# Optimization experiments

Measured on AMD Instinct MI355X. Metric: run time of the kernel, lower is better.

Reference implementation:

```python
import jax, jax.numpy as jnp
import numpy as np

N_GROUPS = 8
TOPK_GROUPS = 4
TOPK = 8
ROUTE_SCALE = 2.5


def setup_inputs() -> dict:
    key = jax.random.key(0)
    k1, k2, k3 = jax.random.split(key, 3)
    x = jax.random.normal(k1, (8192, 7168), dtype=jnp.float32)
    weight = jax.random.normal(k2, (256, 7168), dtype=jnp.float32) * 0.02
    bias = jax.random.normal(k3, (256,), dtype=jnp.float32) * 0.02
    return {"x": x, "weight": weight, "bias": bias}


def reference(x, weight, bias):
    n_tokens = x.shape[0]
    n_experts = weight.shape[0]
    # router GEMM: [T, E]
    logits = jnp.einsum('td,ed->te', x, weight)
    scores = jax.nn.sigmoid(logits)  # score_func == 'sigmoid'
    original_scores = scores
    scores = scores + bias  # bias present since dim == 7168
    # group-limited routing: [T, G, E/G]
    scores_g = scores.reshape(n_tokens, N_GROUPS, -1)
    # bias is not None -> group score = sum of top-2 in each group
    group_scores = jnp.sum(jax.lax.top_k(scores_g, 2)[0], axis=-1)  # [T, G]
    _, grp_idx = jax.lax.top_k(group_scores, TOPK_GROUPS)  # [T, topk_groups]
    mask = jnp.sum(jax.nn.one_hot(grp_idx, N_GROUPS, dtype=scores.dtype), axis=1)  # [T, G]
    masked = (scores_g * mask[:, :, None]).reshape(n_tokens, n_experts)
    _, indices = jax.lax.top_k(masked, TOPK)  # [T, topk]
    weights = jnp.take_along_axis(original_scores, indices, axis=1)
    weights = weights / jnp.sum(weights, axis=-1, keepdims=True)  # sigmoid normalization
    weights = weights * ROUTE_SCALE
    return weights.astype(x.dtype), indices
```

## Files before the change

### kernel.cpp

```cpp
#include <hip/hip_runtime.h>
#include <math.h>

typedef _Float16 f16;
typedef f16 f16x4 __attribute__((ext_vector_type(4)));
typedef f16 f16x8 __attribute__((ext_vector_type(8)));
typedef float f32x4 __attribute__((ext_vector_type(4)));

#define TOKENS 8192
#define EXPERTS 256
#define KDIM 7168
#define BM 128
#define BN 256
#define BK 32
#define SPLITK 4
#define KCHUNK (KDIM / SPLITK)
#define NSTEP (KCHUNK / BK)
#define APAD 40

#define XSCALE 256.0f
#define WSCALE 4096.0f

__device__ __forceinline__ void cvt4(const float4 v, const float scale, f16x4* hi, f16x4* lo) {
  float a = v.x * scale, b = v.y * scale, c = v.z * scale, d = v.w * scale;
  f16 ha = (f16)a, hb = (f16)b, hc = (f16)c, hd = (f16)d;
  f16x4 h, l;
  h.x = ha; h.y = hb; h.z = hc; h.w = hd;
  l.x = (f16)(a - (float)ha);
  l.y = (f16)(b - (float)hb);
  l.z = (f16)(c - (float)hc);
  l.w = (f16)(d - (float)hd);
  *hi = h; *lo = l;
}

__global__ __launch_bounds__(512, 2) void router_gemm(const float* __restrict__ x,
                                                      const float* __restrict__ w,
                                                      float* __restrict__ logits) {
  __shared__ f16 Ah[BM][APAD], Al[BM][APAD];
  __shared__ f16 Bh[BN][APAD], Bl[BN][APAD];

  const int tid = threadIdx.x;
  const int mtile = blockIdx.x >> 2;
  const int ks = blockIdx.x & 3;
  const int m0 = mtile * BM;
  const int k0 = ks * KCHUNK;

  const int lane = tid & 63;
  const int wv = tid >> 6;
  const int wm = wv >> 2;
  const int wn = wv & 3;
  const int fr = lane & 15;
  const int fq = lane >> 4;

  f32x4 acc0[4][4];
  f32x4 accX[4][4];
#pragma unroll
  for (int i = 0; i < 4; ++i)
#pragma unroll
    for (int j = 0; j < 4; ++j) {
      acc0[i][j] = (f32x4){0.f, 0.f, 0.f, 0.f};
      accX[i][j] = (f32x4){0.f, 0.f, 0.f, 0.f};
    }

  const int arow0 = tid >> 3;
  const int ac4 = tid & 7;
  const float* xp = x + (size_t)(m0 + arow0) * KDIM + k0 + ac4 * 4;
  const float* wp = w + (size_t)arow0 * KDIM + k0 + ac4 * 4;

  float4 ra[2], rb[4];
#pragma unroll
  for (int i = 0; i < 2; ++i) ra[i] = *(const float4*)(xp + (size_t)(64 * i) * KDIM);
#pragma unroll
  for (int i = 0; i < 4; ++i) rb[i] = *(const float4*)(wp + (size_t)(64 * i) * KDIM);

  for (int step = 0; step < NSTEP; ++step) {
    __syncthreads();
#pragma unroll
    for (int i = 0; i < 2; ++i) {
      f16x4 h, l;
      cvt4(ra[i], XSCALE, &h, &l);
      const int row = arow0 + 64 * i;
      *(f16x4*)&Ah[row][ac4 * 4] = h;
      *(f16x4*)&Al[row][ac4 * 4] = l;
    }
#pragma unroll
    for (int i = 0; i < 4; ++i) {
      f16x4 h, l;
      cvt4(rb[i], WSCALE, &h, &l);
      const int row = arow0 + 64 * i;
      *(f16x4*)&Bh[row][ac4 * 4] = h;
      *(f16x4*)&Bl[row][ac4 * 4] = l;
    }
    __syncthreads();
    if (step + 1 < NSTEP) {
      const float* xq = xp + (step + 1) * BK;
      const float* wq = wp + (step + 1) * BK;
#pragma unroll
      for (int i = 0; i < 2; ++i) ra[i] = *(const float4*)(xq + (size_t)(64 * i) * KDIM);
#pragma unroll
      for (int i = 0; i < 4; ++i) rb[i] = *(const float4*)(wq + (size_t)(64 * i) * KDIM);
    }
    f16x8 fa_h[4], fa_l[4], fb_h[4], fb_l[4];
#pragma unroll
    for (int m = 0; m < 4; ++m) {
      const int row = wm * 64 + m * 16 + fr;
      fa_h[m] = *(const f16x8*)&Ah[row][fq * 8];
      fa_l[m] = *(const f16x8*)&Al[row][fq * 8];
    }
#pragma unroll
    for (int n = 0; n < 4; ++n) {
      const int row = wn * 64 + n * 16 + fr;
      fb_h[n] = *(const f16x8*)&Bh[row][fq * 8];
      fb_l[n] = *(const f16x8*)&Bl[row][fq * 8];
    }
#pragma unroll
    for (int m = 0; m < 4; ++m)
#pragma unroll
      for (int n = 0; n < 4; ++n) {
        acc0[m][n] = __builtin_amdgcn_mfma_f32_16x16x32_f16(fa_h[m], fb_h[n], acc0[m][n], 0, 0, 0);
        accX[m][n] = __builtin_amdgcn_mfma_f32_16x16x32_f16(fa_h[m], fb_l[n], accX[m][n], 0, 0, 0);
        accX[m][n] = __builtin_amdgcn_mfma_f32_16x16x32_f16(fa_l[m], fb_h[n], accX[m][n], 0, 0, 0);
      }
  }

  constexpr float inv = 1.0f / (XSCALE * WSCALE);
#pragma unroll
  for (int m = 0; m < 4; ++m)
#pragma unroll
    for (int n = 0; n < 4; ++n)
#pragma unroll
      for (int j = 0; j < 4; ++j) {
        const int row = m0 + wm * 64 + m * 16 + fq * 4 + j;
        const int col = wn * 64 + n * 16 + fr;
        atomicAdd(&logits[(size_t)row * EXPERTS + col], (acc0[m][n][j] + accX[m][n][j]) * inv);
      }
}

__global__ __launch_bounds__(256) void router_select(const float* __restrict__ logits,
                                                     const float* __restrict__ bias,
                                                     float* __restrict__ out) {
  const int lane = threadIdx.x & 63;
  const int t = (blockIdx.x << 2) + (threadIdx.x >> 6);

  const float4 lg = reinterpret_cast<const float4*>(logits)[(size_t)t * 64 + lane];
  const float4 bb = reinterpret_cast<const float4*>(bias)[lane];

  const float s0 = (float)(1.0 / (1.0 + exp(-(double)lg.x)));
  const float s1 = (float)(1.0 / (1.0 + exp(-(double)lg.y)));
  const float s2 = (float)(1.0 / (1.0 + exp(-(double)lg.z)));
  const float s3 = (float)(1.0 / (1.0 + exp(-(double)lg.w)));
  const float b0 = s0 + bb.x, b1 = s1 + bb.y, b2 = s2 + bb.z, b3 = s3 + bb.w;

  float v1 = b0, v2 = -1e30f;
  if (b1 > v1) { v2 = v1; v1 = b1; } else if (b1 > v2) v2 = b1;
  if (b2 > v1) { v2 = v1; v1 = b2; } else if (b2 > v2) v2 = b2;
  if (b3 > v1) { v2 = v1; v1 = b3; } else if (b3 > v2) v2 = b3;
#pragma unroll
  for (int d = 1; d < 8; d <<= 1) {
    const float o1 = __shfl_xor(v1, d), o2 = __shfl_xor(v2, d);
    const float n1 = fmaxf(v1, o1);
    const float n2 = fmaxf(fminf(v1, o1), fmaxf(v2, o2));
    v1 = n1; v2 = n2;
  }
  const float gs = v1 + v2;

  const float gv0 = __shfl(gs, 0),  gv1 = __shfl(gs, 8),  gv2 = __shfl(gs, 16), gv3 = __shfl(gs, 24);
  const float gv4 = __shfl(gs, 32), gv5 = __shfl(gs, 40), gv6 = __shfl(gs, 48), gv7 = __shfl(gs, 56);

  unsigned sel = 0;
#pragma unroll
  for (int it = 0; it < 4; ++it) {
    float bvv = -1e30f; int bg = 0;
    if (!(sel & 1u)   && gv0 > bvv) { bvv = gv0; bg = 0; }
    if (!(sel & 2u)   && gv1 > bvv) { bvv = gv1; bg = 1; }
    if (!(sel & 4u)   && gv2 > bvv) { bvv = gv2; bg = 2; }
    if (!(sel & 8u)   && gv3 > bvv) { bvv = gv3; bg = 3; }
    if (!(sel & 16u)  && gv4 > bvv) { bvv = gv4; bg = 4; }
    if (!(sel & 32u)  && gv5 > bvv) { bvv = gv5; bg = 5; }
    if (!(sel & 64u)  && gv6 > bvv) { bvv = gv6; bg = 6; }
    if (!(sel & 128u) && gv7 > bvv) { bvv = gv7; bg = 7; }
    sel |= (1u << bg);
  }

  const bool keep = (sel >> (lane >> 3)) & 1u;
  float c0 = keep ? b0 : -1e30f, c1 = keep ? b1 : -1e30f;
  float c2 = keep ? b2 : -1e30f, c3 = keep ? b3 : -1e30f;

  float wsum = 0.0f, myw = 0.0f;
  int myi = 0;
#pragma unroll
  for (int rnd = 0; rnd < 8; ++rnd) {
    float bv = c0; int bj = 0;
    if (c1 > bv) { bv = c1; bj = 1; }
    if (c2 > bv) { bv = c2; bj = 2; }
    if (c3 > bv) { bv = c3; bj = 3; }
    float bs = (bj == 0) ? s0 : (bj == 1) ? s1 : (bj == 2) ? s2 : s3;
    int bi = (lane << 2) | bj;
#pragma unroll
    for (int d = 1; d < 64; d <<= 1) {
      const float ov = __shfl_xor(bv, d);
      const int oi = __shfl_xor(bi, d);
      const float os = __shfl_xor(bs, d);
      if (ov > bv || (ov == bv && oi < bi)) { bv = ov; bi = oi; bs = os; }
    }
    wsum += bs;
    if (lane == rnd) { myw = bs; myi = bi; }
    if ((bi >> 2) == lane) {
      const int jj = bi & 3;
      if (jj == 0) c0 = -1e30f;
      else if (jj == 1) c1 = -1e30f;
      else if (jj == 2) c2 = -1e30f;
      else c3 = -1e30f;
    }
  }

  if (lane < 8) {
    out[(size_t)t * 8 + lane] = myw * 2.5f / wsum;
    out[(size_t)TOKENS * 8 + (size_t)t * 8 + lane] = (float)myi;
  }
}

extern "C" void kernel_launch(void* const* d_in, const int* in_sizes, int n_in,
                              void* d_out, int out_size, void* d_ws, size_t ws_size,
                              hipStream_t stream) {
  const float* x = (const float*)d_in[0];
  const float* w = (const float*)d_in[1];
  const float* bias = (const float*)d_in[2];
  float* out = (float*)d_out;
  float* logits = (float*)d_ws;

  hipMemsetAsync(logits, 0, (size_t)TOKENS * EXPERTS * sizeof(float), stream);
  router_gemm<<<dim3(64 * SPLITK), dim3(512), 0, stream>>>(x, w, logits);
  router_select<<<dim3(TOKENS / 4), dim3(256), 0, stream>>>(logits, bias, out);
}
```

Measured before the change: 423.8 us.

## Pre-split weights to fp16 hi/lo once and raise split-K to 8

Adds a pre-pass kernel that converts the fp32 weight matrix into fp16 hi and lo arrays in workspace, so the GEMM loads ready-made halves instead of converting the weight tile in every block. Split-K goes from 4 to 8 and launch bounds ask for 4 blocks per SM, giving 512 blocks instead of 256 to fill more CUs. The costs are an extra kernel launch and weight pass, more atomic adds into the logits, and a fallback path when the workspace is too small.

```diff
diff --git a/kernel.cpp b/kernel.cpp
--- a/kernel.cpp
+++ b/kernel.cpp
@@ -12,13 +12,17 @@
 #define BM 128
 #define BN 256
 #define BK 32
-#define SPLITK 4
+#define SPLITK 8
 #define KCHUNK (KDIM / SPLITK)
 #define NSTEP (KCHUNK / BK)
 #define APAD 40
 
 #define XSCALE 256.0f
 #define WSCALE 4096.0f
+
+#define LOGITS_BYTES ((size_t)TOKENS * EXPERTS * 4)
+#define WSPLIT_ELEMS ((size_t)EXPERTS * KDIM)
+#define WS_NEEDED (LOGITS_BYTES + 2 * WSPLIT_ELEMS * 2)
 
 __device__ __forceinline__ void cvt4(const float4 v, const float scale, f16x4* hi, f16x4* lo) {
   float a = v.x * scale, b = v.y * scale, c = v.z * scale, d = v.w * scale;
@@ -32,15 +36,28 @@
   *hi = h; *lo = l;
 }
 
-__global__ __launch_bounds__(512, 2) void router_gemm(const float* __restrict__ x,
+__global__ __launch_bounds__(256) void cvt_w(const float* __restrict__ w,
+                                             f16* __restrict__ wh, f16* __restrict__ wl) {
+  const size_t i = ((size_t)blockIdx.x * 256 + threadIdx.x) * 4;
+  const float4 v = *(const float4*)(w + i);
+  f16x4 h, l;
+  cvt4(v, WSCALE, &h, &l);
+  *(f16x4*)(wh + i) = h;
+  *(f16x4*)(wl + i) = l;
+}
+
+template <bool PRESPLIT>
+__global__ __launch_bounds__(512, 4) void router_gemm(const float* __restrict__ x,
                                                       const float* __restrict__ w,
+                                                      const f16* __restrict__ wh,
+                                                      const f16* __restrict__ wl,
                                                       float* __restrict__ logits) {
   __shared__ f16 Ah[BM][APAD], Al[BM][APAD];
   __shared__ f16 Bh[BN][APAD], Bl[BN][APAD];
 
   const int tid = threadIdx.x;
-  const int mtile = blockIdx.x >> 2;
-  const int ks = blockIdx.x & 3;
+  const int mtile = blockIdx.x >> 3;
+  const int ks = blockIdx.x & 7;
   const int m0 = mtile * BM;
   const int k0 = ks * KCHUNK;
 
@@ -64,13 +81,27 @@
   const int arow0 = tid >> 3;
   const int ac4 = tid & 7;
   const float* xp = x + (size_t)(m0 + arow0) * KDIM + k0 + ac4 * 4;
-  const float* wp = w + (size_t)arow0 * KDIM + k0 + ac4 * 4;
+
+  const int wrow = tid >> 1;
+  const int wseg = (tid & 1) * 16;
+  const f16* whp = wh + (size_t)wrow * KDIM + k0 + wseg;
+  const f16* wlp = wl + (size_t)wrow * KDIM + k0 + wseg;
+  const float* wp = w + (size_t)(tid >> 3) * KDIM + k0 + ac4 * 4;
 
   float4 ra[2], rb[4];
+  f16x8 rbh[2], rbl[2];
 #pragma unroll
   for (int i = 0; i < 2; ++i) ra[i] = *(const float4*)(xp + (size_t)(64 * i) * KDIM);
-#pragma unroll
-  for (int i = 0; i < 4; ++i) rb[i] = *(const float4*)(wp + (size_t)(64 * i) * KDIM);
+  if constexpr (PRESPLIT) {
+#pragma unroll
+    for (int i = 0; i < 2; ++i) {
+      rbh[i] = *(const f16x8*)(whp + 8 * i);
+      rbl[i] = *(const f16x8*)(wlp + 8 * i);
+    }
+  } else {
+#pragma unroll
+    for (int i = 0; i < 4; ++i) rb[i] = *(const float4*)(wp + (size_t)(64 * i) * KDIM);
+  }
 
   for (int step = 0; step < NSTEP; ++step) {
     __syncthreads();
@@ -82,22 +113,38 @@
       *(f16x4*)&Ah[row][ac4 * 4] = h;
       *(f16x4*)&Al[row][ac4 * 4] = l;
     }
-#pragma unroll
-    for (int i = 0; i < 4; ++i) {
-      f16x4 h, l;
-      cvt4(rb[i], WSCALE, &h, &l);
-      const int row = arow0 + 64 * i;
-      *(f16x4*)&Bh[row][ac4 * 4] = h;
-      *(f16x4*)&Bl[row][ac4 * 4] = l;
+    if constexpr (PRESPLIT) {
+#pragma unroll
+      for (int i = 0; i < 2; ++i) {
+        *(f16x8*)&Bh[wrow][wseg + 8 * i] = rbh[i];
+        *(f16x8*)&Bl[wrow][wseg + 8 * i] = rbl[i];
+      }
+    } else {
+#pragma unroll
+      for (int i = 0; i < 4; ++i) {
+        f16x4 h, l;
+        cvt4(rb[i], WSCALE, &h, &l);
+        const int row = (tid >> 3) + 64 * i;
+        *(f16x4*)&Bh[row][ac4 * 4] = h;
+        *(f16x4*)&Bl[row][ac4 * 4] = l;
+      }
     }
     __syncthreads();
     if (step + 1 < NSTEP) {
       const float* xq = xp + (step + 1) * BK;
-      const float* wq = wp + (step + 1) * BK;
 #pragma unroll
       for (int i = 0; i < 2; ++i) ra[i] = *(const float4*)(xq + (size_t)(64 * i) * KDIM);
-#pragma unroll
-      for (int i = 0; i < 4; ++i) rb[i] = *(const float4*)(wq + (size_t)(64 * i) * KDIM);
+      if constexpr (PRESPLIT) {
+#pragma unroll
+        for (int i = 0; i < 2; ++i) {
+          rbh[i] = *(const f16x8*)(whp + (step + 1) * BK + 8 * i);
+          rbl[i] = *(const f16x8*)(wlp + (step + 1) * BK + 8 * i);
+        }
+      } else {
+        const float* wq = wp + (step + 1) * BK;
+#pragma unroll
+        for (int i = 0; i < 4; ++i) rb[i] = *(const float4*)(wq + (size_t)(64 * i) * KDIM);
+      }
     }
     f16x8 fa_h[4], fa_l[4], fb_h[4], fb_l[4];
 #pragma unroll
@@ -227,8 +274,17 @@
   const float* bias = (const float*)d_in[2];
   float* out = (float*)d_out;
   float* logits = (float*)d_ws;
-
-  hipMemsetAsync(logits, 0, (size_t)TOKENS * EXPERTS * sizeof(float), stream);
-  router_gemm<<<dim3(64 * SPLITK), dim3(512), 0, stream>>>(x, w, logits);
+  f16* wh = (f16*)((char*)d_ws + LOGITS_BYTES);
+  f16* wl = wh + WSPLIT_ELEMS;
+
+  const bool presplit = (ws_size >= WS_NEEDED);
+
+  hipMemsetAsync(logits, 0, LOGITS_BYTES, stream);
+  if (presplit) {
+    cvt_w<<<dim3(WSPLIT_ELEMS / (256 * 4)), dim3(256), 0, stream>>>(w, wh, wl);
+    router_gemm<true><<<dim3(64 * SPLITK), dim3(512), 0, stream>>>(x, w, wh, wl, logits);
+  } else {
+    router_gemm<false><<<dim3(64 * SPLITK), dim3(512), 0, stream>>>(x, w, wh, wl, logits);
+  }
   router_select<<<dim3(TOKENS / 4), dim3(256), 0, stream>>>(logits, bias, out);
 }
```

After: 1.136 ms. 168% more time.
